# Kernel tuning notes

Hardware: AMD Instinct MI355X
Metric: run time of the kernel (lower is better)

Reference implementation:

```python
import jax, jax.numpy as jnp
import numpy as np

D_MODEL = 768
NUM_HEADS = 8
HEAD_DIM = D_MODEL // NUM_HEADS


def setup_inputs() -> dict:
    key = jax.random.key(0)
    ks = jax.random.split(key, 5)
    B, N = 4, 2048
    scale = 1.0 / np.sqrt(D_MODEL)
    return {
        "x": jax.random.normal(ks[0], (B, N, D_MODEL), dtype=jnp.float32),
        "W_qkv": jax.random.normal(ks[1], (D_MODEL, 3 * D_MODEL), dtype=jnp.float32) * scale,
        "b_qkv": jax.random.normal(ks[2], (3 * D_MODEL,), dtype=jnp.float32) * 0.01,
        "W_out": jax.random.normal(ks[3], (D_MODEL, D_MODEL), dtype=jnp.float32) * scale,
        "b_out": jax.random.normal(ks[4], (D_MODEL,), dtype=jnp.float32) * 0.01,
    }


def reference(x, W_qkv, b_qkv, W_out, b_out):
    B, N, _ = x.shape
    H, Dh = NUM_HEADS, HEAD_DIM
    # fused QKV projection: [B,N,3*D] -> [3,B,H,N,Dh]
    qkv = (x @ W_qkv + b_qkv).reshape(B, N, 3, H, Dh).transpose(2, 0, 3, 1, 4)
    q, k, v = qkv[0], qkv[1], qkv[2]
    # full NxN attention, as in the original (no masking)
    scores = jnp.einsum("bhnd,bhmd->bhnm", q, k) / jnp.sqrt(jnp.float32(Dh)).astype(x.dtype)
    weights = jax.nn.softmax(scores, axis=-1)
    out = jnp.einsum("bhnm,bhmd->bhnd", weights, v)  # [B,H,N,Dh]
    out = out.transpose(0, 2, 1, 3).reshape(B, N, H * Dh)
    return out @ W_out + b_out
```

## Files before the change

kernel.cpp:

```cpp
#include <hip/hip_runtime.h>
#include <hip/hip_bf16.h>
#include <math.h>

#define BB      4
#define NN      2048
#define DM      768
#define NH      8
#define DHH     96
#define BH      (BB*NH)
#define MROWS   (BB*NN)
#define NC_QKV  (3*DM)

typedef short v8s  __attribute__((ext_vector_type(8)));
typedef float v16f __attribute__((ext_vector_type(16)));

static __device__ __forceinline__ ushort f2bf(float f) {
    __hip_bfloat16 h = __float2bfloat16(f);
    return *reinterpret_cast<ushort*>(&h);
}

static __device__ __forceinline__ void gload_lds16(const ushort* g, ushort* l) {
    __builtin_amdgcn_global_load_lds(
        (const __attribute__((address_space(1))) void*)g,
        (__attribute__((address_space(3))) void*)l, 16, 0, 0);
}

__global__ __launch_bounds__(256)
void conv_bf16(const float* __restrict__ in, ushort* __restrict__ out, int n8)
{
    int i = blockIdx.x * 256 + threadIdx.x;
    if (i >= n8) return;
    const float4* p = reinterpret_cast<const float4*>(in) + (size_t)i * 2;
    float4 a = p[0], b = p[1];
    ushort r[8] = {f2bf(a.x), f2bf(a.y), f2bf(a.z), f2bf(a.w),
                   f2bf(b.x), f2bf(b.y), f2bf(b.z), f2bf(b.w)};
    *reinterpret_cast<v8s*>(out + (size_t)i * 8) = *reinterpret_cast<v8s*>(r);
}

__global__ __launch_bounds__(256)
void convT_bf16(const float* __restrict__ W, ushort* __restrict__ Wt, int K, int N)
{
    __shared__ ushort t[32][33];
    const int k0 = blockIdx.x * 32, n0 = blockIdx.y * 32;
    const int tx = threadIdx.x & 31, ty = threadIdx.x >> 5;
    #pragma unroll
    for (int r = ty; r < 32; r += 8)
        t[tx][r] = f2bf(W[(size_t)(k0 + r) * N + n0 + tx]);
    __syncthreads();
    #pragma unroll
    for (int r = ty; r < 32; r += 8)
        Wt[(size_t)(n0 + r) * K + k0 + tx] = t[r][tx];
}

template<int SCATTER>
__global__ __launch_bounds__(256)
void gemm_mfma(const ushort* __restrict__ A, const ushort* __restrict__ Bt,
               const float* __restrict__ bias, void* __restrict__ outp,
               int K, int Ncols)
{
    __shared__ ushort As[8192];
    __shared__ ushort Bs[8192];

    const int tid  = threadIdx.x;
    const int lane = tid & 63;
    const int wv   = tid >> 6;
    const int l31  = lane & 31;
    const int lhi  = lane >> 5;
    const int wr   = wv >> 1, wc = wv & 1;
    const int row0 = blockIdx.x * 128;
    const int col0 = blockIdx.y * 128;

    v16f acc[2][2];
    #pragma unroll
    for (int mi = 0; mi < 2; ++mi)
        #pragma unroll
        for (int nj = 0; nj < 2; ++nj)
            #pragma unroll
            for (int i = 0; i < 16; ++i) acc[mi][nj][i] = 0.0f;

    for (int k0 = 0; k0 < K; k0 += 64) {
        #pragma unroll
        for (int c = 0; c < 4; ++c) {
            const int idx = (c * 4 + wv) * 64 + lane;
            const int s = idx >> 7, r = idx & 127;
            gload_lds16(&A [(size_t)(row0 + r) * K + k0 + s * 8], &As[(size_t)(c * 4 + wv) * 512]);
            gload_lds16(&Bt[(size_t)(col0 + r) * K + k0 + s * 8], &Bs[(size_t)(c * 4 + wv) * 512]);
        }
        __syncthreads();

        #pragma unroll
        for (int s16 = 0; s16 < 4; ++s16) {
            const int ks = s16 * 2 + lhi;
            v8s a0 = *reinterpret_cast<const v8s*>(&As[(size_t)(ks * 128 + 64 * wr + l31) * 8]);
            v8s a1 = *reinterpret_cast<const v8s*>(&As[(size_t)(ks * 128 + 64 * wr + 32 + l31) * 8]);
            v8s b0 = *reinterpret_cast<const v8s*>(&Bs[(size_t)(ks * 128 + 64 * wc + l31) * 8]);
            v8s b1 = *reinterpret_cast<const v8s*>(&Bs[(size_t)(ks * 128 + 64 * wc + 32 + l31) * 8]);
            acc[0][0] = __builtin_amdgcn_mfma_f32_32x32x16_bf16(a0, b0, acc[0][0], 0, 0, 0);
            acc[0][1] = __builtin_amdgcn_mfma_f32_32x32x16_bf16(a0, b1, acc[0][1], 0, 0, 0);
            acc[1][0] = __builtin_amdgcn_mfma_f32_32x32x16_bf16(a1, b0, acc[1][0], 0, 0, 0);
            acc[1][1] = __builtin_amdgcn_mfma_f32_32x32x16_bf16(a1, b1, acc[1][1], 0, 0, 0);
        }
        __syncthreads();
    }

    #pragma unroll
    for (int nj = 0; nj < 2; ++nj) {
        const int c = col0 + 64 * wc + 32 * nj + l31;
        const float bv = bias[c];
        #pragma unroll
        for (int mi = 0; mi < 2; ++mi) {
            #pragma unroll
            for (int r = 0; r < 16; ++r) {
                const int m = row0 + 64 * wr + 32 * mi + (r & 3) + 8 * (r >> 2) + 4 * lhi;
                const float v = acc[mi][nj][r] + bv;
                if (SCATTER) {
                    const int s   = c / DM;
                    const int rem = c - s * DM;
                    const int h   = rem / DHH;
                    const int d   = rem - h * DHH;
                    const int b   = m >> 11;
                    const int n   = m & (NN - 1);
                    ((ushort*)outp)[((size_t)(s * BH + b * NH + h) * NN + n) * DHH + d] = f2bf(v);
                } else {
                    ((float*)outp)[(size_t)m * Ncols + c] = v;
                }
            }
        }
    }
}

__global__ __launch_bounds__(256)
void attn_mfma(const ushort* __restrict__ qkv, ushort* __restrict__ attnout)
{
    __shared__ ushort Ks[64][104];
    __shared__ ushort Vt[96][72];
    __shared__ ushort Ps[4][32][72];

    const int tid  = threadIdx.x;
    const int lane = tid & 63;
    const int wv   = tid >> 6;
    const int l31  = lane & 31;
    const int lhi  = lane >> 5;
    const int q0   = blockIdx.x * 128;
    const int bh   = blockIdx.y;
    const int b    = bh >> 3, h = bh & 7;

    const ushort* Qg = qkv + (size_t)bh * NN * DHH;
    const ushort* Kg = qkv + ((size_t)BH + bh) * NN * DHH;
    const ushort* Vg = qkv + ((size_t)2 * BH + bh) * NN * DHH;

    const int qr = q0 + wv * 32 + l31;
    v8s qf[6];
    #pragma unroll
    for (int kt = 0; kt < 6; ++kt)
        qf[kt] = *reinterpret_cast<const v8s*>(&Qg[(size_t)qr * DHH + kt * 16 + lhi * 8]);

    v16f o[3];
    #pragma unroll
    for (int dt = 0; dt < 3; ++dt)
        #pragma unroll
        for (int i = 0; i < 16; ++i) o[dt][i] = 0.0f;
    float dsum[16];
    #pragma unroll
    for (int r = 0; r < 16; ++r) dsum[r] = 0.0f;

    const float sc = 0.14724599350930152f;

    for (int kt0 = 0; kt0 < NN; kt0 += 64) {
        #pragma unroll
        for (int it = 0; it < 3; ++it) {
            int idx = it * 256 + tid;
            int r = idx / 12, cc = (idx - r * 12) * 8;
            *reinterpret_cast<v8s*>(&Ks[r][cc]) =
                *reinterpret_cast<const v8s*>(&Kg[(size_t)(kt0 + r) * DHH + cc]);
        }
        #pragma unroll
        for (int it = 0; it < 3; ++it) {
            int c8 = (it * 4 + wv) * 8;
            v8s vv = *reinterpret_cast<const v8s*>(&Vg[(size_t)(kt0 + lane) * DHH + c8]);
            #pragma unroll
            for (int j = 0; j < 8; ++j) Vt[c8 + j][lane] = (ushort)vv[j];
        }
        __syncthreads();

        #pragma unroll
        for (int ct = 0; ct < 2; ++ct) {
            v16f s;
            #pragma unroll
            for (int i = 0; i < 16; ++i) s[i] = 0.0f;
            #pragma unroll
            for (int kt = 0; kt < 6; ++kt) {
                v8s kf = *reinterpret_cast<const v8s*>(&Ks[ct * 32 + l31][kt * 16 + lhi * 8]);
                s = __builtin_amdgcn_mfma_f32_32x32x16_bf16(qf[kt], kf, s, 0, 0, 0);
            }
            #pragma unroll
            for (int r = 0; r < 16; ++r) {
                float e = exp2f(s[r] * sc);
                dsum[r] += e;
                int qrow = (r & 3) + 8 * (r >> 2) + 4 * lhi;
                Ps[wv][qrow][ct * 32 + l31] = f2bf(e);
            }
        }

        v8s pa[4];
        #pragma unroll
        for (int ks = 0; ks < 4; ++ks)
            pa[ks] = *reinterpret_cast<const v8s*>(&Ps[wv][l31][ks * 16 + lhi * 8]);
        #pragma unroll
        for (int dt = 0; dt < 3; ++dt) {
            #pragma unroll
            for (int ks = 0; ks < 4; ++ks) {
                v8s vb = *reinterpret_cast<const v8s*>(&Vt[dt * 32 + l31][ks * 16 + lhi * 8]);
                o[dt] = __builtin_amdgcn_mfma_f32_32x32x16_bf16(pa[ks], vb, o[dt], 0, 0, 0);
            }
        }
        __syncthreads();
    }

    #pragma unroll
    for (int r = 0; r < 16; ++r) {
        float d = dsum[r];
        #pragma unroll
        for (int off = 1; off < 32; off <<= 1) d += __shfl_xor(d, off, 64);
        dsum[r] = 1.0f / d;
    }

    #pragma unroll
    for (int dt = 0; dt < 3; ++dt) {
        #pragma unroll
        for (int r = 0; r < 16; ++r) {
            int qrow = (r & 3) + 8 * (r >> 2) + 4 * lhi;
            int n = q0 + wv * 32 + qrow;
            attnout[((size_t)(b * NN + n)) * DM + h * DHH + dt * 32 + l31] =
                f2bf(o[dt][r] * dsum[r]);
        }
    }
}

extern "C" void kernel_launch(void* const* d_in, const int* in_sizes, int n_in,
                              void* d_out, int out_size, void* d_ws, size_t ws_size,
                              hipStream_t stream)
{
    (void)in_sizes; (void)n_in; (void)out_size; (void)ws_size;
    const float* x    = (const float*)d_in[0];
    const float* Wqkv = (const float*)d_in[1];
    const float* bqkv = (const float*)d_in[2];
    const float* Wout = (const float*)d_in[3];
    const float* bout = (const float*)d_in[4];
    float* out = (float*)d_out;

    ushort* qkv   = (ushort*)d_ws;
    ushort* ao    = qkv   + (size_t)3 * BH * NN * DHH;
    ushort* xbf   = ao    + (size_t)MROWS * DM;
    ushort* wqkvt = xbf   + (size_t)MROWS * DM;
    ushort* woutt = wqkvt + (size_t)DM * NC_QKV;

    dim3 blk(256);

    conv_bf16<<<dim3(MROWS * DM / 8 / 256), blk, 0, stream>>>(x, xbf, MROWS * DM / 8);
    convT_bf16<<<dim3(DM / 32, NC_QKV / 32), blk, 0, stream>>>(Wqkv, wqkvt, DM, NC_QKV);
    convT_bf16<<<dim3(DM / 32, DM / 32), blk, 0, stream>>>(Wout, woutt, DM, DM);

    gemm_mfma<1><<<dim3(MROWS / 128, NC_QKV / 128), blk, 0, stream>>>(
        xbf, wqkvt, bqkv, (void*)qkv, DM, NC_QKV);

    attn_mfma<<<dim3(NN / 128, BH), blk, 0, stream>>>(qkv, ao);

    gemm_mfma<0><<<dim3(MROWS / 128, DM / 128), blk, 0, stream>>>(
        ao, woutt, bout, (void*)out, DM, DM);
}
```

Measured before the change: 214.4 us.

## Double-buffer K/V tiles, keep P in registers via transposed MFMA, fold Q scale

The attention kernel now double-buffers the K and V shared-memory tiles, prefetching the next tile into registers while computing the current one, so only one barrier is needed per iteration. It computes S^T = K·Q^T so each lane owns one query row, and builds the P fragment in registers with cross-half shuffles instead of a round trip through shared memory. The row-sum reduction shrinks to a single shuffle, and the output is written as packed 8-byte stores. The softmax scale is folded into Q in the QKV projection epilogue, which removes a multiply per score but also rounds the scaled Q to bf16, a small accuracy change.

```diff
diff --git a/kernel.cpp b/kernel.cpp
--- a/kernel.cpp
+++ b/kernel.cpp
@@ -13,6 +13,9 @@
 
 typedef short v8s  __attribute__((ext_vector_type(8)));
 typedef float v16f __attribute__((ext_vector_type(16)));
+typedef unsigned int u32;
+
+#define SCQ 0.14724599350930152f
 
 static __device__ __forceinline__ ushort f2bf(float f) {
     __hip_bfloat16 h = __float2bfloat16(f);
@@ -23,6 +26,12 @@
     __builtin_amdgcn_global_load_lds(
         (const __attribute__((address_space(1))) void*)g,
         (__attribute__((address_space(3))) void*)l, 16, 0, 0);
+}
+
+static __device__ __forceinline__ v8s pack_frag(u32 a, u32 b, u32 c, u32 d) {
+    union { u32 u[4]; v8s s; } x;
+    x.u[0] = a; x.u[1] = b; x.u[2] = c; x.u[3] = d;
+    return x.s;
 }
 
 __global__ __launch_bounds__(256)
@@ -112,7 +121,7 @@
             #pragma unroll
             for (int r = 0; r < 16; ++r) {
                 const int m = row0 + 64 * wr + 32 * mi + (r & 3) + 8 * (r >> 2) + 4 * lhi;
-                const float v = acc[mi][nj][r] + bv;
+                float v = acc[mi][nj][r] + bv;
                 if (SCATTER) {
                     const int s   = c / DM;
                     const int rem = c - s * DM;
@@ -120,6 +129,7 @@
                     const int d   = rem - h * DHH;
                     const int b   = m >> 11;
                     const int n   = m & (NN - 1);
+                    if (s == 0) v *= SCQ;
                     ((ushort*)outp)[((size_t)(s * BH + b * NH + h) * NN + n) * DHH + d] = f2bf(v);
                 } else {
                     ((float*)outp)[(size_t)m * Ncols + c] = v;
@@ -132,9 +142,8 @@
 __global__ __launch_bounds__(256)
 void attn_mfma(const ushort* __restrict__ qkv, ushort* __restrict__ attnout)
 {
-    __shared__ ushort Ks[64][104];
-    __shared__ ushort Vt[96][72];
-    __shared__ ushort Ps[4][32][72];
+    __shared__ ushort Ks[2][6144];
+    __shared__ ushort Vt[2][96][72];
 
     const int tid  = threadIdx.x;
     const int lane = tid & 63;
@@ -160,29 +169,42 @@
     for (int dt = 0; dt < 3; ++dt)
         #pragma unroll
         for (int i = 0; i < 16; ++i) o[dt][i] = 0.0f;
-    float dsum[16];
-    #pragma unroll
-    for (int r = 0; r < 16; ++r) dsum[r] = 0.0f;
-
-    const float sc = 0.14724599350930152f;
-
-    for (int kt0 = 0; kt0 < NN; kt0 += 64) {
-        #pragma unroll
-        for (int it = 0; it < 3; ++it) {
-            int idx = it * 256 + tid;
-            int r = idx / 12, cc = (idx - r * 12) * 8;
-            *reinterpret_cast<v8s*>(&Ks[r][cc]) =
-                *reinterpret_cast<const v8s*>(&Kg[(size_t)(kt0 + r) * DHH + cc]);
-        }
-        #pragma unroll
-        for (int it = 0; it < 3; ++it) {
-            int c8 = (it * 4 + wv) * 8;
-            v8s vv = *reinterpret_cast<const v8s*>(&Vg[(size_t)(kt0 + lane) * DHH + c8]);
-            #pragma unroll
-            for (int j = 0; j < 8; ++j) Vt[c8 + j][lane] = (ushort)vv[j];
-        }
-        __syncthreads();
-
+    float dsum = 0.0f;
+
+    {
+        v8s kr[3], vr[3];
+        #pragma unroll
+        for (int i = 0; i < 3; ++i) {
+            kr[i] = *reinterpret_cast<const v8s*>(&Kg[(size_t)lane * DHH + (wv * 3 + i) * 8]);
+            vr[i] = *reinterpret_cast<const v8s*>(&Vg[(size_t)lane * DHH + (i * 4 + wv) * 8]);
+        }
+        #pragma unroll
+        for (int i = 0; i < 3; ++i) {
+            *reinterpret_cast<v8s*>(&Ks[0][(wv * 3 + i) * 512 + lane * 8]) = kr[i];
+            #pragma unroll
+            for (int j = 0; j < 8; ++j)
+                Vt[0][(i * 4 + wv) * 8 + j][lane] = (ushort)vr[i][j];
+        }
+    }
+    __syncthreads();
+
+    for (int t = 0; t < 32; ++t) {
+        const int cur = t & 1, nxt = cur ^ 1;
+        const int kbase = (t + 1) * 64;
+
+        v8s kr0, kr1, kr2, vr0, vr1, vr2;
+        if (t < 31) {
+            const ushort* krow = &Kg[(size_t)(kbase + lane) * DHH];
+            const ushort* vrow = &Vg[(size_t)(kbase + lane) * DHH];
+            kr0 = *reinterpret_cast<const v8s*>(&krow[(wv * 3 + 0) * 8]);
+            kr1 = *reinterpret_cast<const v8s*>(&krow[(wv * 3 + 1) * 8]);
+            kr2 = *reinterpret_cast<const v8s*>(&krow[(wv * 3 + 2) * 8]);
+            vr0 = *reinterpret_cast<const v8s*>(&vrow[(0 * 4 + wv) * 8]);
+            vr1 = *reinterpret_cast<const v8s*>(&vrow[(1 * 4 + wv) * 8]);
+            vr2 = *reinterpret_cast<const v8s*>(&vrow[(2 * 4 + wv) * 8]);
+        }
+
+        v8s pfrag[4];
         #pragma unroll
         for (int ct = 0; ct < 2; ++ct) {
             v16f s;
@@ -190,49 +212,68 @@
             for (int i = 0; i < 16; ++i) s[i] = 0.0f;
             #pragma unroll
             for (int kt = 0; kt < 6; ++kt) {
-                v8s kf = *reinterpret_cast<const v8s*>(&Ks[ct * 32 + l31][kt * 16 + lhi * 8]);
-                s = __builtin_amdgcn_mfma_f32_32x32x16_bf16(qf[kt], kf, s, 0, 0, 0);
+                v8s kf = *reinterpret_cast<const v8s*>(
+                    &Ks[cur][((kt * 2 + lhi) * 64 + ct * 32 + l31) * 8]);
+                s = __builtin_amdgcn_mfma_f32_32x32x16_bf16(kf, qf[kt], s, 0, 0, 0);
             }
+            float e[16];
             #pragma unroll
             for (int r = 0; r < 16; ++r) {
-                float e = exp2f(s[r] * sc);
-                dsum[r] += e;
-                int qrow = (r & 3) + 8 * (r >> 2) + 4 * lhi;
-                Ps[wv][qrow][ct * 32 + l31] = f2bf(e);
+                e[r] = exp2f(s[r]);
+                dsum += e[r];
             }
-        }
-
-        v8s pa[4];
-        #pragma unroll
-        for (int ks = 0; ks < 4; ++ks)
-            pa[ks] = *reinterpret_cast<const v8s*>(&Ps[wv][l31][ks * 16 + lhi * 8]);
+            u32 w[8];
+            #pragma unroll
+            for (int i = 0; i < 8; ++i)
+                w[i] = (u32)f2bf(e[2 * i]) | ((u32)f2bf(e[2 * i + 1]) << 16);
+            const u32 t0 = __shfl_xor(lhi ? w[0] : w[2], 32, 64);
+            const u32 t1 = __shfl_xor(lhi ? w[1] : w[3], 32, 64);
+            const u32 t2 = __shfl_xor(lhi ? w[4] : w[6], 32, 64);
+            const u32 t3 = __shfl_xor(lhi ? w[5] : w[7], 32, 64);
+            pfrag[2 * ct + 0] = lhi ? pack_frag(t0, t1, w[2], w[3])
+                                    : pack_frag(w[0], w[1], t0, t1);
+            pfrag[2 * ct + 1] = lhi ? pack_frag(t2, t3, w[6], w[7])
+                                    : pack_frag(w[4], w[5], t2, t3);
+        }
+
         #pragma unroll
         for (int dt = 0; dt < 3; ++dt) {
             #pragma unroll
             for (int ks = 0; ks < 4; ++ks) {
-                v8s vb = *reinterpret_cast<const v8s*>(&Vt[dt * 32 + l31][ks * 16 + lhi * 8]);
-                o[dt] = __builtin_amdgcn_mfma_f32_32x32x16_bf16(pa[ks], vb, o[dt], 0, 0, 0);
+                v8s va = *reinterpret_cast<const v8s*>(
+                    &Vt[cur][dt * 32 + l31][ks * 16 + lhi * 8]);
+                o[dt] = __builtin_amdgcn_mfma_f32_32x32x16_bf16(va, pfrag[ks], o[dt], 0, 0, 0);
             }
         }
+
+        if (t < 31) {
+            *reinterpret_cast<v8s*>(&Ks[nxt][(wv * 3 + 0) * 512 + lane * 8]) = kr0;
+            *reinterpret_cast<v8s*>(&Ks[nxt][(wv * 3 + 1) * 512 + lane * 8]) = kr1;
+            *reinterpret_cast<v8s*>(&Ks[nxt][(wv * 3 + 2) * 512 + lane * 8]) = kr2;
+            #pragma unroll
+            for (int j = 0; j < 8; ++j) Vt[nxt][(0 * 4 + wv) * 8 + j][lane] = (ushort)vr0[j];
+            #pragma unroll
+            for (int j = 0; j < 8; ++j) Vt[nxt][(1 * 4 + wv) * 8 + j][lane] = (ushort)vr1[j];
+            #pragma unroll
+            for (int j = 0; j < 8; ++j) Vt[nxt][(2 * 4 + wv) * 8 + j][lane] = (ushort)vr2[j];
+        }
         __syncthreads();
     }
 
-    #pragma unroll
-    for (int r = 0; r < 16; ++r) {
-        float d = dsum[r];
-        #pragma unroll
-        for (int off = 1; off < 32; off <<= 1) d += __shfl_xor(d, off, 64);
-        dsum[r] = 1.0f / d;
-    }
-
+    dsum += __shfl_xor(dsum, 32, 64);
+    const float inv = 1.0f / dsum;
+
+    const int n = q0 + wv * 32 + l31;
+    ushort* orow = attnout + ((size_t)(b * NN + n)) * DM + h * DHH;
     #pragma unroll
     for (int dt = 0; dt < 3; ++dt) {
         #pragma unroll
-        for (int r = 0; r < 16; ++r) {
-            int qrow = (r & 3) + 8 * (r >> 2) + 4 * lhi;
-            int n = q0 + wv * 32 + qrow;
-            attnout[((size_t)(b * NN + n)) * DM + h * DHH + dt * 32 + l31] =
-                f2bf(o[dt][r] * dsum[r]);
+        for (int g = 0; g < 4; ++g) {
+            const int d0 = dt * 32 + 8 * g + 4 * lhi;
+            u32 w0 = (u32)f2bf(o[dt][4 * g + 0] * inv) | ((u32)f2bf(o[dt][4 * g + 1] * inv) << 16);
+            u32 w1 = (u32)f2bf(o[dt][4 * g + 2] * inv) | ((u32)f2bf(o[dt][4 * g + 3] * inv) << 16);
+            uint2 pk; pk.x = w0; pk.y = w1;
+            *reinterpret_cast<uint2*>(&orow[d0]) = pk;
         }
     }
 }
```

Result: faster. 208.3 us (-2.9%).
